# Kernel optimization log

Hardware: AMD Instinct MI355X
Metric: run time of the kernel (lower is better)

Reference implementation:

```python
import jax, jax.numpy as jnp
import numpy as np

D_MODEL = 1024
N_SEQ = 2048
H = 16


def _rope_tables(d, n_seq):
    # theta_i = 10000^(-2i/d), i in [0, d/2)
    i = jnp.arange(d // 2, dtype=jnp.float32)
    theta = jnp.power(10000.0, -2.0 * i / d)                 # [d/2]
    ang = jnp.arange(n_seq, dtype=jnp.float32)[:, None] * theta[None, :]  # [S, d/2]
    cos = jnp.repeat(jnp.cos(ang), 2, axis=-1)               # [S, d] (cos duplicated per pair)
    s = jnp.sin(ang)
    sin = jnp.stack([s, -s], axis=-1).reshape(n_seq, d)      # [S, d] (+sin, -sin interleaved)
    return cos, sin


def _apply_rope(x, cos, sin):
    d = x.shape[-1]
    # swap adjacent pairs: (x0,x1,x2,x3,...) -> (x1,x0,x3,x2,...)
    x2 = x.reshape(x.shape[:-1] + (d // 2, 2))[..., ::-1].reshape(x.shape)
    return x * cos + x2 * sin


def setup_inputs() -> dict:
    key = jax.random.key(0)
    ks = jax.random.split(key, 8)
    B, S, D = 2, N_SEQ, D_MODEL
    scale = 1.0 / np.sqrt(D)
    return {
        "q": jax.random.normal(ks[0], (B, S, D), dtype=jnp.float32),
        "k": jax.random.normal(ks[1], (B, S, D), dtype=jnp.float32),
        "v": jax.random.normal(ks[2], (B, S, D), dtype=jnp.float32),
        "W_q": jax.random.normal(ks[3], (D, D), dtype=jnp.float32) * scale,
        "W_k": jax.random.normal(ks[4], (D, D), dtype=jnp.float32) * scale,
        "W_v": jax.random.normal(ks[5], (D, D), dtype=jnp.float32) * scale,
        "W_o": jax.random.normal(ks[6], (D, D), dtype=jnp.float32) * scale,
        "b_o": jax.random.normal(ks[7], (D,), dtype=jnp.float32) * scale,
    }


def reference(q, k, v, W_q, W_k, W_v, W_o, b_o):
    B, S, D = q.shape
    d_k = D // H
    cos, sin = _rope_tables(D, N_SEQ)

    query = _apply_rope(q @ W_q.T, cos, sin)  # RoPE over full d_model, pre head-split
    key_ = _apply_rope(k @ W_k.T, cos, sin)
    value = v @ W_v.T

    def split_heads(x):
        return x.reshape(B, S, H, d_k).transpose(0, 2, 1, 3)  # [B,H,S,dk]

    qh, kh, vh = split_heads(query), split_heads(key_), split_heads(value)

    scores = jnp.einsum("bhsd,bhtd->bhst", qh, kh) / jnp.sqrt(jnp.float32(d_k))
    attn = jax.nn.softmax(scores, axis=-1)
    y = jnp.einsum("bhst,bhtd->bhsd", attn, vh)               # [B,H,S,dk]
    y = y.transpose(0, 2, 1, 3).reshape(B, S, D)
    return y @ W_o.T + b_o
```

## Files before the change

### kernel.cpp

```cpp
#include <hip/hip_runtime.h>
#include <hip/hip_bf16.h>

using bf16 = __hip_bfloat16;
using bf16x8 = __attribute__((ext_vector_type(8))) short;
using f32x4 = __attribute__((ext_vector_type(4))) float;

#define LOG2E 1.44269504088896f

__device__ __forceinline__ void gload_lds16(const void* g, void* lds) {
    __builtin_amdgcn_global_load_lds(
        (const __attribute__((address_space(1))) void*)g,
        (__attribute__((address_space(3))) void*)lds, 16, 0, 0);
}

struct __align__(16) BH8 { bf16 h[8]; };
struct __align__(8)  BH4 { bf16 h[4]; };

struct CvtArgs { const float* src[7]; BH8* dst[7]; };

__global__ __launch_bounds__(256) void cvt_all(CvtArgs ca) {
    int i = blockIdx.x * 256 + threadIdx.x;
    const float* src; BH8* dst; int off;
    if (i < 3 * 524288) {
        int w = i >> 19; off = i & 524287;
        src = ca.src[w]; dst = ca.dst[w];
    } else {
        int j = i - 3 * 524288;
        int w = 3 + (j >> 17); off = j & 131071;
        src = ca.src[w]; dst = ca.dst[w];
    }
    const float4* p = (const float4*)src + (size_t)off * 2;
    float4 a = p[0], b = p[1];
    BH8 r;
    r.h[0] = __float2bfloat16(a.x); r.h[1] = __float2bfloat16(a.y);
    r.h[2] = __float2bfloat16(a.z); r.h[3] = __float2bfloat16(a.w);
    r.h[4] = __float2bfloat16(b.x); r.h[5] = __float2bfloat16(b.y);
    r.h[6] = __float2bfloat16(b.z); r.h[7] = __float2bfloat16(b.w);
    dst[off] = r;
}

__global__ __launch_bounds__(256) void rope_tables(float* __restrict__ ct,
                                                   float* __restrict__ st) {
    int idx = blockIdx.x * 256 + threadIdx.x;
    if (idx >= 2048 * 512) return;
    int s = idx >> 9, i = idx & 511;
    float theta = exp2f((float)i * -0.0259525632413075f);
    float ang = (float)s * theta;
    ct[idx] = cosf(ang);
    st[idx] = sinf(ang);
}

struct ProjArgs {
    const bf16* A[3];
    const bf16* W[3];
    void* out[3];
    int mode[3];
};

template <int MF>
__global__ __launch_bounds__(256, 2) void gemm_bt(ProjArgs pa,
        const float* __restrict__ ct, const float* __restrict__ st,
        const float* __restrict__ bias) {
    constexpr int Kd = 1024;
    constexpr int BM = MF * 32;
    __shared__ __align__(16) bf16 As[BM * 32];
    __shared__ __align__(16) bf16 Bs[128 * 32];
    const int z = blockIdx.z;
    const bf16* __restrict__ A = pa.A[z];
    const bf16* __restrict__ W = pa.W[z];
    const int mode = pa.mode[z];
    const int tid = threadIdx.x, wid = tid >> 6, lane = tid & 63;
    const int g = lane >> 4, l15 = lane & 15;
    const int wm = wid >> 1, wn = wid & 1;
    const int m0 = blockIdx.y * BM, n0 = blockIdx.x * 128;
    f32x4 acc[MF][4] = {};
    const int sbyte = wid * 1024 + lane * 16;

    for (int kb = 0; kb < Kd; kb += 32) {
        __syncthreads();
#pragma unroll
        for (int r = 0; r < MF / 2; ++r) {
            int byte = sbyte + r * 4096;
            int row = byte >> 6, cb = byte & 63;
            int csrc = cb ^ (((row >> 1) & 3) << 4);
            gload_lds16((const char*)(A + (size_t)(m0 + row) * Kd + kb) + csrc,
                        (char*)As + wid * 1024 + r * 4096);
        }
#pragma unroll
        for (int r = 0; r < 2; ++r) {
            int byte = sbyte + r * 4096;
            int row = byte >> 6, cb = byte & 63;
            int csrc = cb ^ (((row >> 1) & 3) << 4);
            gload_lds16((const char*)(W + (size_t)(n0 + row) * Kd + kb) + csrc,
                        (char*)Bs + wid * 1024 + r * 4096);
        }
        __syncthreads();
        bf16x8 af[MF], bw[4];
#pragma unroll
        for (int i = 0; i < MF; ++i) {
            int ra = wm * (MF * 16) + i * 16 + l15;
            af[i] = *(const bf16x8*)((const char*)As + ra * 64 +
                                     ((g * 16) ^ (((ra >> 1) & 3) << 4)));
        }
#pragma unroll
        for (int j = 0; j < 4; ++j) {
            int rb = wn * 64 + j * 16 + l15;
            bw[j] = *(const bf16x8*)((const char*)Bs + rb * 64 +
                                     ((g * 16) ^ (((rb >> 1) & 3) << 4)));
        }
#pragma unroll
        for (int i = 0; i < MF; ++i)
#pragma unroll
            for (int j = 0; j < 4; ++j)
                acc[i][j] = __builtin_amdgcn_mfma_f32_16x16x32_bf16(af[i], bw[j], acc[i][j], 0, 0, 0);
    }

    if (mode == 0) {
        float* out = (float*)pa.out[z];
#pragma unroll
        for (int i = 0; i < MF; ++i) {
            int row = m0 + wm * (MF * 16) + i * 16 + g * 4;
#pragma unroll
            for (int j = 0; j < 4; ++j) {
                int col = n0 + wn * 64 + j * 16 + l15;
                float bv = bias[col];
#pragma unroll
                for (int r = 0; r < 4; ++r)
                    out[(size_t)(row + r) * 1024 + col] = acc[i][j][r] + bv;
            }
        }
    } else if (mode == 3) {
        bf16* out = (bf16*)pa.out[z];
#pragma unroll
        for (int i = 0; i < MF; ++i) {
            int m = m0 + wm * (MF * 16) + i * 16 + g * 4;
            int b = m >> 11, s = m & 2047;
#pragma unroll
            for (int j = 0; j < 4; ++j) {
                int col = n0 + wn * 64 + j * 16 + l15;
                int h = col >> 6, dv = col & 63;
                BH4 pk;
#pragma unroll
                for (int r = 0; r < 4; ++r) pk.h[r] = __float2bfloat16(acc[i][j][r]);
                *(BH4*)(out + (((size_t)(b * 16 + h)) * 64 + dv) * 2048 + s) = pk;
            }
        }
    } else {
        bf16* out = (bf16*)pa.out[z];
        float scl = (mode == 1) ? (0.125f * LOG2E) : 1.0f;
#pragma unroll
        for (int i = 0; i < MF; ++i) {
            int mrow = m0 + wm * (MF * 16) + i * 16 + g * 4;
#pragma unroll
            for (int j = 0; j < 4; ++j) {
                int col = n0 + wn * 64 + j * 16 + l15;
                int ci = col >> 1;
                float sgn = (col & 1) ? -1.0f : 1.0f;
                int h = col >> 6, dv = col & 63;
#pragma unroll
                for (int r = 0; r < 4; ++r) {
                    int m = mrow + r;
                    int b = m >> 11, s = m & 2047;
                    float vv = acc[i][j][r];
                    float pv = __shfl_xor(vv, 1);
                    float c = ct[s * 512 + ci], sn = st[s * 512 + ci];
                    float o = (vv * c + sgn * sn * pv) * scl;
                    out[(((size_t)(b * 16 + h)) * 2048 + s) * 64 + dv] = __float2bfloat16(o);
                }
            }
        }
    }
}

__global__ __launch_bounds__(128, 2) void attn_fwd(
        const bf16* __restrict__ Qh, const bf16* __restrict__ Kh,
        const bf16* __restrict__ Vt, bf16* __restrict__ Y) {
    __shared__ __align__(16) bf16 Ks[2][64 * 64];
    __shared__ __align__(16) bf16 Vs[2][64 * 64];
    const int tid = threadIdx.x, wid = tid >> 6, lane = tid & 63;
    const int g = lane >> 4, l15 = lane & 15;
    const int lin = blockIdx.y * 32 + blockIdx.x;
    const int swz = (lin & 7) * 128 + (lin >> 3);
    const int bh = swz >> 5, qt = swz & 31;
    const int q0 = qt * 64 + wid * 32;
    const bf16* Qb = Qh + (size_t)bh * 2048 * 64;
    const bf16* Kb = Kh + (size_t)bh * 2048 * 64;
    const bf16* Vb = Vt + (size_t)bh * 64 * 2048;

    bf16x8 aq[2][2];
#pragma unroll
    for (int qfr = 0; qfr < 2; ++qfr)
#pragma unroll
        for (int kk = 0; kk < 2; ++kk)
            aq[qfr][kk] = *(const bf16x8*)(Qb + (size_t)(q0 + qfr * 16 + l15) * 64 + kk * 32 + g * 8);

    f32x4 yacc[2][4] = {};
    float lrow[2] = {0.f, 0.f};

    int srow[4], csrc[4], kphys[4];
#pragma unroll
    for (int i = 0; i < 4; ++i) {
        int byte = wid * 1024 + lane * 16 + i * 2048;
        srow[i] = byte >> 7;
        csrc[i] = (byte & 127) ^ ((srow[i] & 7) << 4);
        int L = srow[i];
        kphys[i] = ((L >> 5) << 5) + (((L >> 2) & 3) << 3) + (((L >> 4) & 1) << 2) + (L & 3);
    }

#define STAGE(T, BUF)                                                           \
    do {                                                                        \
        _Pragma("unroll")                                                       \
        for (int i = 0; i < 4; ++i) {                                           \
            gload_lds16((const char*)(Kb + (size_t)((T) * 64 + kphys[i]) * 64) + csrc[i], \
                        (char*)&Ks[BUF][0] + wid * 1024 + i * 2048);            \
            gload_lds16((const char*)(Vb + (size_t)srow[i] * 2048 + (T) * 64) + csrc[i],  \
                        (char*)&Vs[BUF][0] + wid * 1024 + i * 2048);            \
        }                                                                       \
    } while (0)

    STAGE(0, 0);

    for (int t = 0; t < 32; ++t) {
        __syncthreads();
        if (t < 31) STAGE(t + 1, (t + 1) & 1);
        const char* Kst = (const char*)&Ks[t & 1][0];
        const char* Vst = (const char*)&Vs[t & 1][0];

        f32x4 sacc[4][2] = {};
#pragma unroll
        for (int kk = 0; kk < 2; ++kk) {
            bf16x8 kf[4];
#pragma unroll
            for (int kfr = 0; kfr < 4; ++kfr)
                kf[kfr] = *(const bf16x8*)(Kst + (kfr * 16 + l15) * 128 +
                                           ((kk * 64 + g * 16) ^ ((l15 & 7) << 4)));
#pragma unroll
            for (int kfr = 0; kfr < 4; ++kfr)
#pragma unroll
                for (int qfr = 0; qfr < 2; ++qfr)
                    sacc[kfr][qfr] = __builtin_amdgcn_mfma_f32_16x16x32_bf16(
                        kf[kfr], aq[qfr][kk], sacc[kfr][qfr], 0, 0, 0);
        }

        bf16x8 ap[2][2];
#pragma unroll
        for (int qfr = 0; qfr < 2; ++qfr)
#pragma unroll
            for (int ch = 0; ch < 2; ++ch) {
                bf16 hh[8];
#pragma unroll
                for (int r = 0; r < 4; ++r) {
                    float x = exp2f(sacc[2 * ch][qfr][r]);
                    lrow[qfr] += x;
                    hh[r] = __float2bfloat16(x);
                }
#pragma unroll
                for (int r = 0; r < 4; ++r) {
                    float x = exp2f(sacc[2 * ch + 1][qfr][r]);
                    lrow[qfr] += x;
                    hh[4 + r] = __float2bfloat16(x);
                }
                ap[qfr][ch] = *(const bf16x8*)hh;
            }

#pragma unroll
        for (int ch = 0; ch < 2; ++ch) {
            bf16x8 bv[4];
#pragma unroll
            for (int dn = 0; dn < 4; ++dn)
                bv[dn] = *(const bf16x8*)(Vst + (dn * 16 + l15) * 128 +
                                          ((ch * 64 + g * 16) ^ ((l15 & 7) << 4)));
#pragma unroll
            for (int qfr = 0; qfr < 2; ++qfr)
#pragma unroll
                for (int dn = 0; dn < 4; ++dn)
                    yacc[qfr][dn] = __builtin_amdgcn_mfma_f32_16x16x32_bf16(
                        ap[qfr][ch], bv[dn], yacc[qfr][dn], 0, 0, 0);
        }
    }
#undef STAGE

    const int b = bh >> 4, h = bh & 15;
#pragma unroll
    for (int qfr = 0; qfr < 2; ++qfr) {
        float ls = lrow[qfr];
        ls += __shfl_xor(ls, 16);
        ls += __shfl_xor(ls, 32);
#pragma unroll
        for (int r = 0; r < 4; ++r) {
            float lv = __shfl(ls, g * 4 + r);
            float inv = 1.0f / lv;
            int s = q0 + qfr * 16 + g * 4 + r;
            bf16* yp = Y + ((size_t)(b * 2048 + s)) * 1024 + h * 64;
#pragma unroll
            for (int dn = 0; dn < 4; ++dn)
                yp[dn * 16 + l15] = __float2bfloat16(yacc[qfr][dn][r] * inv);
        }
    }
}

extern "C" void kernel_launch(void* const* d_in, const int* in_sizes, int n_in,
                              void* d_out, int out_size, void* d_ws, size_t ws_size,
                              hipStream_t stream) {
    const float* q  = (const float*)d_in[0];
    const float* k  = (const float*)d_in[1];
    const float* v  = (const float*)d_in[2];
    const float* Wq = (const float*)d_in[3];
    const float* Wk = (const float*)d_in[4];
    const float* Wv = (const float*)d_in[5];
    const float* Wo = (const float*)d_in[6];
    const float* bo = (const float*)d_in[7];

    const size_t MB = 1048576ull;
    if (ws_size < 72 * MB) return;
    char* p = (char*)d_ws;
    bf16* qb  = (bf16*)(p + 0 * MB);
    bf16* kb  = (bf16*)(p + 8 * MB);
    bf16* vb  = (bf16*)(p + 16 * MB);
    bf16* Wqb = (bf16*)(p + 24 * MB);
    bf16* Wkb = (bf16*)(p + 26 * MB);
    bf16* Wvb = (bf16*)(p + 28 * MB);
    bf16* Wob = (bf16*)(p + 30 * MB);
    bf16* Qh  = (bf16*)(p + 32 * MB);
    bf16* Kh  = (bf16*)(p + 40 * MB);
    bf16* Vt  = (bf16*)(p + 48 * MB);
    bf16* Yb  = (bf16*)(p + 56 * MB);
    float* ct = (float*)(p + 64 * MB);
    float* st = (float*)(p + 68 * MB);

    CvtArgs ca;
    ca.src[0] = q;  ca.dst[0] = (BH8*)qb;
    ca.src[1] = k;  ca.dst[1] = (BH8*)kb;
    ca.src[2] = v;  ca.dst[2] = (BH8*)vb;
    ca.src[3] = Wq; ca.dst[3] = (BH8*)Wqb;
    ca.src[4] = Wk; ca.dst[4] = (BH8*)Wkb;
    ca.src[5] = Wv; ca.dst[5] = (BH8*)Wvb;
    ca.src[6] = Wo; ca.dst[6] = (BH8*)Wob;
    cvt_all<<<8192, 256, 0, stream>>>(ca);
    rope_tables<<<4096, 256, 0, stream>>>(ct, st);

    ProjArgs pa;
    pa.A[0] = qb;  pa.A[1] = kb;  pa.A[2] = vb;
    pa.W[0] = Wqb; pa.W[1] = Wkb; pa.W[2] = Wvb;
    pa.out[0] = Qh; pa.out[1] = Kh; pa.out[2] = Vt;
    pa.mode[0] = 1; pa.mode[1] = 2; pa.mode[2] = 3;
    gemm_bt<4><<<dim3(8, 32, 3), 256, 0, stream>>>(pa, ct, st, nullptr);

    attn_fwd<<<dim3(32, 32), 128, 0, stream>>>(Qh, Kh, Vt, Yb);

    ProjArgs pf;
    pf.A[0] = Yb; pf.A[1] = Yb; pf.A[2] = Yb;
    pf.W[0] = Wob; pf.W[1] = Wob; pf.W[2] = Wob;
    pf.out[0] = d_out; pf.out[1] = d_out; pf.out[2] = d_out;
    pf.mode[0] = 0; pf.mode[1] = 0; pf.mode[2] = 0;
    gemm_bt<2><<<dim3(8, 64, 1), 256, 0, stream>>>(pf, ct, st, bo);
}
```

Measured before the change: 150.2 us.

## Compute softmax row sums via MFMA with ones, packed bf16 convert, MFMA priority

Softmax denominators are now accumulated by an extra MFMA of the bf16 probability tile against a ones vector, replacing per-lane scalar adds and the cross-lane shuffles in the epilogue. The exp results are packed to bf16 with v_cvt_pk_bf16_f32 inline asm instead of per-element conversions. s_setprio is raised around the MFMA blocks to favour matrix issue across waves. The row sums are now taken from bf16-rounded probabilities, which matches what is fed to the PV product but changes rounding slightly. The extra MFMAs add matrix-pipe work.

```diff
diff --git a/kernel.cpp b/kernel.cpp
--- a/kernel.cpp
+++ b/kernel.cpp
@@ -194,8 +194,12 @@
         for (int kk = 0; kk < 2; ++kk)
             aq[qfr][kk] = *(const bf16x8*)(Qb + (size_t)(q0 + qfr * 16 + l15) * 64 + kk * 32 + g * 8);
 
+    bf16x8 ones;
+#pragma unroll
+    for (int i = 0; i < 8; ++i) ones[i] = (short)0x3F80;
+
     f32x4 yacc[2][4] = {};
-    float lrow[2] = {0.f, 0.f};
+    f32x4 lacc[2] = {};
 
     int srow[4], csrc[4], kphys[4];
 #pragma unroll
@@ -234,12 +238,14 @@
             for (int kfr = 0; kfr < 4; ++kfr)
                 kf[kfr] = *(const bf16x8*)(Kst + (kfr * 16 + l15) * 128 +
                                            ((kk * 64 + g * 16) ^ ((l15 & 7) << 4)));
+            __builtin_amdgcn_s_setprio(1);
 #pragma unroll
             for (int kfr = 0; kfr < 4; ++kfr)
 #pragma unroll
                 for (int qfr = 0; qfr < 2; ++qfr)
                     sacc[kfr][qfr] = __builtin_amdgcn_mfma_f32_16x16x32_bf16(
                         kf[kfr], aq[qfr][kk], sacc[kfr][qfr], 0, 0, 0);
+            __builtin_amdgcn_s_setprio(0);
         }
 
         bf16x8 ap[2][2];
@@ -247,20 +253,22 @@
         for (int qfr = 0; qfr < 2; ++qfr)
 #pragma unroll
             for (int ch = 0; ch < 2; ++ch) {
-                bf16 hh[8];
-#pragma unroll
-                for (int r = 0; r < 4; ++r) {
-                    float x = exp2f(sacc[2 * ch][qfr][r]);
-                    lrow[qfr] += x;
-                    hh[r] = __float2bfloat16(x);
-                }
-#pragma unroll
-                for (int r = 0; r < 4; ++r) {
-                    float x = exp2f(sacc[2 * ch + 1][qfr][r]);
-                    lrow[qfr] += x;
-                    hh[4 + r] = __float2bfloat16(x);
-                }
-                ap[qfr][ch] = *(const bf16x8*)hh;
+                float e0 = exp2f(sacc[2 * ch][qfr][0]);
+                float e1 = exp2f(sacc[2 * ch][qfr][1]);
+                float e2 = exp2f(sacc[2 * ch][qfr][2]);
+                float e3 = exp2f(sacc[2 * ch][qfr][3]);
+                float f0 = exp2f(sacc[2 * ch + 1][qfr][0]);
+                float f1 = exp2f(sacc[2 * ch + 1][qfr][1]);
+                float f2 = exp2f(sacc[2 * ch + 1][qfr][2]);
+                float f3 = exp2f(sacc[2 * ch + 1][qfr][3]);
+                union { unsigned int w[4]; bf16x8 v; } u;
+                asm("v_cvt_pk_bf16_f32 %0, %1, %2" : "=v"(u.w[0]) : "v"(e0), "v"(e1));
+                asm("v_cvt_pk_bf16_f32 %0, %1, %2" : "=v"(u.w[1]) : "v"(e2), "v"(e3));
+                asm("v_cvt_pk_bf16_f32 %0, %1, %2" : "=v"(u.w[2]) : "v"(f0), "v"(f1));
+                asm("v_cvt_pk_bf16_f32 %0, %1, %2" : "=v"(u.w[3]) : "v"(f2), "v"(f3));
+                ap[qfr][ch] = u.v;
+                lacc[qfr] = __builtin_amdgcn_mfma_f32_16x16x32_bf16(
+                    ap[qfr][ch], ones, lacc[qfr], 0, 0, 0);
             }
 
 #pragma unroll
@@ -270,12 +278,14 @@
             for (int dn = 0; dn < 4; ++dn)
                 bv[dn] = *(const bf16x8*)(Vst + (dn * 16 + l15) * 128 +
                                           ((ch * 64 + g * 16) ^ ((l15 & 7) << 4)));
+            __builtin_amdgcn_s_setprio(1);
 #pragma unroll
             for (int qfr = 0; qfr < 2; ++qfr)
 #pragma unroll
                 for (int dn = 0; dn < 4; ++dn)
                     yacc[qfr][dn] = __builtin_amdgcn_mfma_f32_16x16x32_bf16(
                         ap[qfr][ch], bv[dn], yacc[qfr][dn], 0, 0, 0);
+            __builtin_amdgcn_s_setprio(0);
         }
     }
 #undef STAGE
@@ -283,13 +293,9 @@
     const int b = bh >> 4, h = bh & 15;
 #pragma unroll
     for (int qfr = 0; qfr < 2; ++qfr) {
-        float ls = lrow[qfr];
-        ls += __shfl_xor(ls, 16);
-        ls += __shfl_xor(ls, 32);
 #pragma unroll
         for (int r = 0; r < 4; ++r) {
-            float lv = __shfl(ls, g * 4 + r);
-            float inv = 1.0f / lv;
+            float inv = 1.0f / lacc[qfr][r];
             int s = q0 + qfr * 16 + g * 4 + r;
             bf16* yp = Y + ((size_t)(b * 2048 + s)) * 1024 + h * 64;
 #pragma unroll
```

After: 150.8 us. No clear change (+0.4%).

## Restructure attention to one-wave blocks with direct V register loads; fuse cvt and rope

Applied to the files above, without the earlier changes.

The attention kernel now runs one 64-thread wave per block over 32 query rows. It drops the __syncthreads barrier and the LDS staging of V. V fragments are loaded straight from global memory into registers each tile, with explicit vmcnt waits to order them against the async K-to-LDS loads. The bf16 conversion and RoPE table kernels are also merged into one launch to save a kernel launch. The risks are more global traffic for V without sharing across waves, and fragile hand-written waitcnt counts.

```diff
diff --git a/kernel.cpp b/kernel.cpp
--- a/kernel.cpp
+++ b/kernel.cpp
@@ -18,36 +18,37 @@
 
 struct CvtArgs { const float* src[7]; BH8* dst[7]; };
 
-__global__ __launch_bounds__(256) void cvt_all(CvtArgs ca) {
-    int i = blockIdx.x * 256 + threadIdx.x;
-    const float* src; BH8* dst; int off;
-    if (i < 3 * 524288) {
-        int w = i >> 19; off = i & 524287;
-        src = ca.src[w]; dst = ca.dst[w];
+__global__ __launch_bounds__(256) void cvt_rope(CvtArgs ca,
+        float* __restrict__ ct, float* __restrict__ st) {
+    int bid = blockIdx.x;
+    if (bid < 8192) {
+        int i = bid * 256 + threadIdx.x;
+        const float* src; BH8* dst; int off;
+        if (i < 3 * 524288) {
+            int w = i >> 19; off = i & 524287;
+            src = ca.src[w]; dst = ca.dst[w];
+        } else {
+            int j = i - 3 * 524288;
+            int w = 3 + (j >> 17); off = j & 131071;
+            src = ca.src[w]; dst = ca.dst[w];
+        }
+        const float4* p = (const float4*)src + (size_t)off * 2;
+        float4 a = p[0], b = p[1];
+        BH8 r;
+        r.h[0] = __float2bfloat16(a.x); r.h[1] = __float2bfloat16(a.y);
+        r.h[2] = __float2bfloat16(a.z); r.h[3] = __float2bfloat16(a.w);
+        r.h[4] = __float2bfloat16(b.x); r.h[5] = __float2bfloat16(b.y);
+        r.h[6] = __float2bfloat16(b.z); r.h[7] = __float2bfloat16(b.w);
+        dst[off] = r;
     } else {
-        int j = i - 3 * 524288;
-        int w = 3 + (j >> 17); off = j & 131071;
-        src = ca.src[w]; dst = ca.dst[w];
-    }
-    const float4* p = (const float4*)src + (size_t)off * 2;
-    float4 a = p[0], b = p[1];
-    BH8 r;
-    r.h[0] = __float2bfloat16(a.x); r.h[1] = __float2bfloat16(a.y);
-    r.h[2] = __float2bfloat16(a.z); r.h[3] = __float2bfloat16(a.w);
-    r.h[4] = __float2bfloat16(b.x); r.h[5] = __float2bfloat16(b.y);
-    r.h[6] = __float2bfloat16(b.z); r.h[7] = __float2bfloat16(b.w);
-    dst[off] = r;
-}
-
-__global__ __launch_bounds__(256) void rope_tables(float* __restrict__ ct,
-                                                   float* __restrict__ st) {
-    int idx = blockIdx.x * 256 + threadIdx.x;
-    if (idx >= 2048 * 512) return;
-    int s = idx >> 9, i = idx & 511;
-    float theta = exp2f((float)i * -0.0259525632413075f);
-    float ang = (float)s * theta;
-    ct[idx] = cosf(ang);
-    st[idx] = sinf(ang);
+        int idx = (bid - 8192) * 256 + threadIdx.x;
+        if (idx >= 2048 * 512) return;
+        int s = idx >> 9, i = idx & 511;
+        float theta = exp2f((float)i * -0.0259525632413075f);
+        float ang = (float)s * theta;
+        ct[idx] = cosf(ang);
+        st[idx] = sinf(ang);
+    }
 }
 
 struct ProjArgs {
@@ -172,17 +173,16 @@
     }
 }
 
-__global__ __launch_bounds__(128, 2) void attn_fwd(
+__global__ __launch_bounds__(64, 2) void attn_fwd(
         const bf16* __restrict__ Qh, const bf16* __restrict__ Kh,
         const bf16* __restrict__ Vt, bf16* __restrict__ Y) {
     __shared__ __align__(16) bf16 Ks[2][64 * 64];
-    __shared__ __align__(16) bf16 Vs[2][64 * 64];
-    const int tid = threadIdx.x, wid = tid >> 6, lane = tid & 63;
+    const int lane = threadIdx.x & 63;
     const int g = lane >> 4, l15 = lane & 15;
-    const int lin = blockIdx.y * 32 + blockIdx.x;
-    const int swz = (lin & 7) * 128 + (lin >> 3);
-    const int bh = swz >> 5, qt = swz & 31;
-    const int q0 = qt * 64 + wid * 32;
+    const int lin = blockIdx.x;
+    const int swz = (lin & 7) * 256 + (lin >> 3);
+    const int bh = swz >> 6, qt = swz & 63;
+    const int q0 = qt * 32;
     const bf16* Qb = Qh + (size_t)bh * 2048 * 64;
     const bf16* Kb = Kh + (size_t)bh * 2048 * 64;
     const bf16* Vb = Vt + (size_t)bh * 64 * 2048;
@@ -197,34 +197,40 @@
     f32x4 yacc[2][4] = {};
     float lrow[2] = {0.f, 0.f};
 
-    int srow[4], csrc[4], kphys[4];
-#pragma unroll
-    for (int i = 0; i < 4; ++i) {
-        int byte = wid * 1024 + lane * 16 + i * 2048;
-        srow[i] = byte >> 7;
-        csrc[i] = (byte & 127) ^ ((srow[i] & 7) << 4);
-        int L = srow[i];
-        kphys[i] = ((L >> 5) << 5) + (((L >> 2) & 3) << 3) + (((L >> 4) & 1) << 2) + (L & 3);
-    }
-
-#define STAGE(T, BUF)                                                           \
-    do {                                                                        \
-        _Pragma("unroll")                                                       \
-        for (int i = 0; i < 4; ++i) {                                           \
-            gload_lds16((const char*)(Kb + (size_t)((T) * 64 + kphys[i]) * 64) + csrc[i], \
-                        (char*)&Ks[BUF][0] + wid * 1024 + i * 2048);            \
-            gload_lds16((const char*)(Vb + (size_t)srow[i] * 2048 + (T) * 64) + csrc[i],  \
-                        (char*)&Vs[BUF][0] + wid * 1024 + i * 2048);            \
-        }                                                                       \
+    int csrc[8], kph[8];
+#pragma unroll
+    for (int i = 0; i < 8; ++i) {
+        int byte = lane * 16 + i * 1024;
+        int L = byte >> 7;
+        csrc[i] = (byte & 127) ^ ((L & 7) << 4);
+        kph[i] = ((L >> 5) << 5) + (((L >> 2) & 3) << 3) + (((L >> 4) & 1) << 2) + (L & 3);
+    }
+
+#define STAGE(T, BUF)                                                          \
+    do {                                                                       \
+        _Pragma("unroll")                                                      \
+        for (int i = 0; i < 8; ++i)                                            \
+            gload_lds16((const char*)(Kb + (size_t)((T) * 64 + kph[i]) * 64) + csrc[i], \
+                        (char*)&Ks[BUF][0] + i * 1024);                        \
     } while (0)
 
     STAGE(0, 0);
 
     for (int t = 0; t < 32; ++t) {
-        __syncthreads();
-        if (t < 31) STAGE(t + 1, (t + 1) & 1);
+        bf16x8 vf[4][2];
+#pragma unroll
+        for (int dn = 0; dn < 4; ++dn)
+#pragma unroll
+            for (int ch = 0; ch < 2; ++ch)
+                vf[dn][ch] = *(const bf16x8*)(Vb + (size_t)(dn * 16 + l15) * 2048 +
+                                              t * 64 + ch * 32 + g * 8);
+        if (t < 31) {
+            STAGE(t + 1, (t + 1) & 1);
+            asm volatile("s_waitcnt vmcnt(16)" ::: "memory");
+        } else {
+            asm volatile("s_waitcnt vmcnt(8)" ::: "memory");
+        }
         const char* Kst = (const char*)&Ks[t & 1][0];
-        const char* Vst = (const char*)&Vs[t & 1][0];
 
         f32x4 sacc[4][2] = {};
 #pragma unroll
@@ -264,19 +270,13 @@
             }
 
 #pragma unroll
-        for (int ch = 0; ch < 2; ++ch) {
-            bf16x8 bv[4];
-#pragma unroll
-            for (int dn = 0; dn < 4; ++dn)
-                bv[dn] = *(const bf16x8*)(Vst + (dn * 16 + l15) * 128 +
-                                          ((ch * 64 + g * 16) ^ ((l15 & 7) << 4)));
+        for (int ch = 0; ch < 2; ++ch)
 #pragma unroll
             for (int qfr = 0; qfr < 2; ++qfr)
 #pragma unroll
                 for (int dn = 0; dn < 4; ++dn)
                     yacc[qfr][dn] = __builtin_amdgcn_mfma_f32_16x16x32_bf16(
-                        ap[qfr][ch], bv[dn], yacc[qfr][dn], 0, 0, 0);
-        }
+                        ap[qfr][ch], vf[dn][ch], yacc[qfr][dn], 0, 0, 0);
     }
 #undef STAGE
 
@@ -336,8 +336,7 @@
     ca.src[4] = Wk; ca.dst[4] = (BH8*)Wkb;
     ca.src[5] = Wv; ca.dst[5] = (BH8*)Wvb;
     ca.src[6] = Wo; ca.dst[6] = (BH8*)Wob;
-    cvt_all<<<8192, 256, 0, stream>>>(ca);
-    rope_tables<<<4096, 256, 0, stream>>>(ct, st);
+    cvt_rope<<<12288, 256, 0, stream>>>(ca, ct, st);
 
     ProjArgs pa;
     pa.A[0] = qb;  pa.A[1] = kb;  pa.A[2] = vb;
@@ -346,7 +345,7 @@
     pa.mode[0] = 1; pa.mode[1] = 2; pa.mode[2] = 3;
     gemm_bt<4><<<dim3(8, 32, 3), 256, 0, stream>>>(pa, ct, st, nullptr);
 
-    attn_fwd<<<dim3(32, 32), 128, 0, stream>>>(Qh, Kh, Vt, Yb);
+    attn_fwd<<<2048, 64, 0, stream>>>(Qh, Kh, Vt, Yb);
 
     ProjArgs pf;
     pf.A[0] = Yb; pf.A[1] = Yb; pf.A[2] = Yb;
```

New measurement: 169.8 us. 1.13x slower.

## Double GEMM K-tile to 64 and merge cvt with rope-table kernel

Applied to the files above, without the earlier changes.

The projection GEMM now stages 64-wide K slices per iteration instead of 32, with a new 128-byte-row XOR swizzle, and issues two MFMA k-steps per barrier pair. This halves the number of sync and loop iterations but doubles LDS use per block, which may reduce occupancy. Separately, the fp32-to-bf16 conversion and RoPE table generation are fused into one launch to save a kernel launch.

```diff
diff --git a/kernel.cpp b/kernel.cpp
--- a/kernel.cpp
+++ b/kernel.cpp
@@ -18,36 +18,37 @@
 
 struct CvtArgs { const float* src[7]; BH8* dst[7]; };
 
-__global__ __launch_bounds__(256) void cvt_all(CvtArgs ca) {
-    int i = blockIdx.x * 256 + threadIdx.x;
-    const float* src; BH8* dst; int off;
-    if (i < 3 * 524288) {
-        int w = i >> 19; off = i & 524287;
-        src = ca.src[w]; dst = ca.dst[w];
+__global__ __launch_bounds__(256) void cvt_rope(CvtArgs ca,
+        float* __restrict__ ct, float* __restrict__ st) {
+    int bid = blockIdx.x;
+    if (bid < 8192) {
+        int i = bid * 256 + threadIdx.x;
+        const float* src; BH8* dst; int off;
+        if (i < 3 * 524288) {
+            int w = i >> 19; off = i & 524287;
+            src = ca.src[w]; dst = ca.dst[w];
+        } else {
+            int j = i - 3 * 524288;
+            int w = 3 + (j >> 17); off = j & 131071;
+            src = ca.src[w]; dst = ca.dst[w];
+        }
+        const float4* p = (const float4*)src + (size_t)off * 2;
+        float4 a = p[0], b = p[1];
+        BH8 r;
+        r.h[0] = __float2bfloat16(a.x); r.h[1] = __float2bfloat16(a.y);
+        r.h[2] = __float2bfloat16(a.z); r.h[3] = __float2bfloat16(a.w);
+        r.h[4] = __float2bfloat16(b.x); r.h[5] = __float2bfloat16(b.y);
+        r.h[6] = __float2bfloat16(b.z); r.h[7] = __float2bfloat16(b.w);
+        dst[off] = r;
     } else {
-        int j = i - 3 * 524288;
-        int w = 3 + (j >> 17); off = j & 131071;
-        src = ca.src[w]; dst = ca.dst[w];
-    }
-    const float4* p = (const float4*)src + (size_t)off * 2;
-    float4 a = p[0], b = p[1];
-    BH8 r;
-    r.h[0] = __float2bfloat16(a.x); r.h[1] = __float2bfloat16(a.y);
-    r.h[2] = __float2bfloat16(a.z); r.h[3] = __float2bfloat16(a.w);
-    r.h[4] = __float2bfloat16(b.x); r.h[5] = __float2bfloat16(b.y);
-    r.h[6] = __float2bfloat16(b.z); r.h[7] = __float2bfloat16(b.w);
-    dst[off] = r;
-}
-
-__global__ __launch_bounds__(256) void rope_tables(float* __restrict__ ct,
-                                                   float* __restrict__ st) {
-    int idx = blockIdx.x * 256 + threadIdx.x;
-    if (idx >= 2048 * 512) return;
-    int s = idx >> 9, i = idx & 511;
-    float theta = exp2f((float)i * -0.0259525632413075f);
-    float ang = (float)s * theta;
-    ct[idx] = cosf(ang);
-    st[idx] = sinf(ang);
+        int idx = (bid - 8192) * 256 + threadIdx.x;
+        if (idx >= 2048 * 512) return;
+        int s = idx >> 9, i = idx & 511;
+        float theta = exp2f((float)i * -0.0259525632413075f);
+        float ang = (float)s * theta;
+        ct[idx] = cosf(ang);
+        st[idx] = sinf(ang);
+    }
 }
 
 struct ProjArgs {
@@ -63,8 +64,8 @@
         const float* __restrict__ bias) {
     constexpr int Kd = 1024;
     constexpr int BM = MF * 32;
-    __shared__ __align__(16) bf16 As[BM * 32];
-    __shared__ __align__(16) bf16 Bs[128 * 32];
+    __shared__ __align__(16) bf16 As[BM * 64];
+    __shared__ __align__(16) bf16 Bs[128 * 64];
     const int z = blockIdx.z;
     const bf16* __restrict__ A = pa.A[z];
     const bf16* __restrict__ W = pa.W[z];
@@ -74,45 +75,53 @@
     const int wm = wid >> 1, wn = wid & 1;
     const int m0 = blockIdx.y * BM, n0 = blockIdx.x * 128;
     f32x4 acc[MF][4] = {};
-    const int sbyte = wid * 1024 + lane * 16;
-
-    for (int kb = 0; kb < Kd; kb += 32) {
+
+    const int sbyte = tid * 16;
+
+    for (int kb = 0; kb < Kd; kb += 64) {
         __syncthreads();
 #pragma unroll
-        for (int r = 0; r < MF / 2; ++r) {
-            int byte = sbyte + r * 4096;
-            int row = byte >> 6, cb = byte & 63;
-            int csrc = cb ^ (((row >> 1) & 3) << 4);
+        for (int i = 0; i < MF; ++i) {
+            int byte = sbyte + i * 4096;
+            int row = byte >> 7, cb = byte & 127;
+            int csrc = cb ^ ((row & 7) << 4);
             gload_lds16((const char*)(A + (size_t)(m0 + row) * Kd + kb) + csrc,
-                        (char*)As + wid * 1024 + r * 4096);
-        }
-#pragma unroll
-        for (int r = 0; r < 2; ++r) {
-            int byte = sbyte + r * 4096;
-            int row = byte >> 6, cb = byte & 63;
-            int csrc = cb ^ (((row >> 1) & 3) << 4);
+                        (char*)As + wid * 1024 + i * 4096);
+        }
+#pragma unroll
+        for (int i = 0; i < 4; ++i) {
+            int byte = sbyte + i * 4096;
+            int row = byte >> 7, cb = byte & 127;
+            int csrc = cb ^ ((row & 7) << 4);
             gload_lds16((const char*)(W + (size_t)(n0 + row) * Kd + kb) + csrc,
-                        (char*)Bs + wid * 1024 + r * 4096);
+                        (char*)Bs + wid * 1024 + i * 4096);
         }
         __syncthreads();
-        bf16x8 af[MF], bw[4];
+        bf16x8 af[MF][2], bw[4][2];
 #pragma unroll
         for (int i = 0; i < MF; ++i) {
             int ra = wm * (MF * 16) + i * 16 + l15;
-            af[i] = *(const bf16x8*)((const char*)As + ra * 64 +
-                                     ((g * 16) ^ (((ra >> 1) & 3) << 4)));
+#pragma unroll
+            for (int kk = 0; kk < 2; ++kk)
+                af[i][kk] = *(const bf16x8*)((const char*)As + ra * 128 +
+                                             ((kk * 64 + g * 16) ^ ((ra & 7) << 4)));
         }
 #pragma unroll
         for (int j = 0; j < 4; ++j) {
             int rb = wn * 64 + j * 16 + l15;
-            bw[j] = *(const bf16x8*)((const char*)Bs + rb * 64 +
-                                     ((g * 16) ^ (((rb >> 1) & 3) << 4)));
-        }
-#pragma unroll
-        for (int i = 0; i < MF; ++i)
-#pragma unroll
-            for (int j = 0; j < 4; ++j)
-                acc[i][j] = __builtin_amdgcn_mfma_f32_16x16x32_bf16(af[i], bw[j], acc[i][j], 0, 0, 0);
+#pragma unroll
+            for (int kk = 0; kk < 2; ++kk)
+                bw[j][kk] = *(const bf16x8*)((const char*)Bs + rb * 128 +
+                                             ((kk * 64 + g * 16) ^ ((rb & 7) << 4)));
+        }
+#pragma unroll
+        for (int kk = 0; kk < 2; ++kk)
+#pragma unroll
+            for (int i = 0; i < MF; ++i)
+#pragma unroll
+                for (int j = 0; j < 4; ++j)
+                    acc[i][j] = __builtin_amdgcn_mfma_f32_16x16x32_bf16(
+                        af[i][kk], bw[j][kk], acc[i][j], 0, 0, 0);
     }
 
     if (mode == 0) {
@@ -336,8 +345,7 @@
     ca.src[4] = Wk; ca.dst[4] = (BH8*)Wkb;
     ca.src[5] = Wv; ca.dst[5] = (BH8*)Wvb;
     ca.src[6] = Wo; ca.dst[6] = (BH8*)Wob;
-    cvt_all<<<8192, 256, 0, stream>>>(ca);
-    rope_tables<<<4096, 256, 0, stream>>>(ct, st);
+    cvt_rope<<<12288, 256, 0, stream>>>(ca, ct, st);
 
     ProjArgs pa;
     pa.A[0] = qb;  pa.A[1] = kb;  pa.A[2] = vb;
```

New measurement: 150.9 us (median of 2 runs). No clear change (+0.5%).
